# Performance work log

Measured on AMD Instinct MI355X. Metric: run time of the kernel, lower is better.

Reference implementation:

```python
import jax, jax.numpy as jnp
import numpy as np
from jax import lax

TAU = 0.1
N_ITERS = 20
B, N = 2048, 256


def setup_inputs() -> dict:
    key = jax.random.key(0)
    k1, k2 = jax.random.split(key)
    x = jax.random.normal(k1, (B, N), dtype=jnp.float32)
    x_norm = jax.random.normal(k2, (B, N), dtype=jnp.float32)
    reference_vec = jnp.linspace(-1.0, 1.0, N, dtype=jnp.float32)
    return {"x": x, "x_norm": x_norm, "reference_vec": reference_vec}


def reference(x, x_norm, reference_vec):
    # log_alpha: [B, N, N] = -|x_norm_i - ref_j| / tau
    log_alpha = -jnp.abs(x_norm[..., None] - reference_vec) / TAU

    def body(la, _):
        la = la - jax.nn.logsumexp(la, axis=-1, keepdims=True)  # row norm
        la = la - jax.nn.logsumexp(la, axis=-2, keepdims=True)  # col norm
        return la, None

    log_alpha, _ = lax.scan(body, log_alpha, None, length=N_ITERS)
    perm = jnp.exp(log_alpha)  # soft permutation [B, N, N]
    return jnp.einsum("bij,bj->bi", perm, x)
```

## Files before the change

### kernel.cpp

```cpp
#include <hip/hip_runtime.h>

#define NN 256
#define NITER 20
static constexpr float KK = 14.426950408889634f;

template<int CTRL, int RM>
__device__ __forceinline__ float dppadd(float x) {
  int v = __builtin_amdgcn_update_dpp(0, __float_as_int(x), CTRL, RM, 0xF, true);
  return x + __int_as_float(v);
}
template<int CTRL, int RM>
__device__ __forceinline__ int dppaddi(int x) {
  int v = __builtin_amdgcn_update_dpp(0, x, CTRL, RM, 0xF, true);
  return x + v;
}
__device__ __forceinline__ float rlane(float v, int l) {
  return __int_as_float(__builtin_amdgcn_readlane(__float_as_int(v), l));
}
__device__ __forceinline__ float rcpf(float x) {
  float r; asm("v_rcp_f32 %0, %1" : "=v"(r) : "v"(x)); return r;
}

__global__ __launch_bounds__(64)
void sinkhorn_wave(const float* __restrict__ x,
                   const float* __restrict__ xn,
                   const float* __restrict__ refv,
                   float* __restrict__ out)
{
  __shared__ __align__(16) float2   W[258];
  __shared__ __align__(16) unsigned hist[NN];
  __shared__ __align__(16) int      exclArr[NN];
  __shared__ __align__(16) float    xsArr[NN];
  __shared__ __align__(16) int      origArr[NN];

  const int lane = threadIdx.x;
  const int b = blockIdx.x;
  const int j4 = lane * 4;
  const size_t base = (size_t)b * NN;

  float xnv[4], xv[4], rv[4];
  { float4 t = *(const float4*)(xn + base + j4); xnv[0]=t.x; xnv[1]=t.y; xnv[2]=t.z; xnv[3]=t.w; }
  { float4 t = *(const float4*)(x  + base + j4); xv[0]=t.x;  xv[1]=t.y;  xv[2]=t.z;  xv[3]=t.w; }
  { float4 t = *(const float4*)(refv + j4);      rv[0]=t.x;  rv[1]=t.y;  rv[2]=t.z;  rv[3]=t.w; }

  *(uint4*)&hist[j4] = make_uint4(0u, 0u, 0u, 0u);
  float vc[4]; int cb[4]; unsigned rtn[4];
  #pragma unroll
  for (int t = 0; t < 4; ++t) {
    vc[t] = fminf(fmaxf(xnv[t], -1.0f), 1.0f);
    cb[t] = (int)fmaf(vc[t], 127.5f, 127.5f);
    rtn[t] = atomicAdd(&hist[cb[t]], 1u);
  }
  uint4 hv = *(uint4*)&hist[j4];
  int ih0 = (int)hv.x, ih1 = ih0 + (int)hv.y, ih2 = ih1 + (int)hv.z, ih3 = ih2 + (int)hv.w;
  int sH = ih3;
  sH = dppaddi<0x111, 0xF>(sH);
  sH = dppaddi<0x112, 0xF>(sH);
  sH = dppaddi<0x114, 0xF>(sH);
  sH = dppaddi<0x118, 0xF>(sH);
  sH = dppaddi<0x142, 0xA>(sH);
  sH = dppaddi<0x143, 0xC>(sH);
  const int offH = sH - ih3;
  int slotM[4] = { offH, offH + ih0, offH + ih1, offH + ih2 };
  *(int4*)&exclArr[j4] = make_int4(slotM[0], slotM[1], slotM[2], slotM[3]);
  #pragma unroll
  for (int t = 0; t < 4; ++t) {
    int slot = exclArr[cb[t]] + (int)rtn[t];
    xsArr[slot]   = vc[t];
    origArr[slot] = j4 + t;
  }
  float xs[4]; int orig[4];
  { float4 t = *(float4*)&xsArr[j4]; xs[0]=t.x; xs[1]=t.y; xs[2]=t.z; xs[3]=t.w; }
  { int4  t = *(int4*)&origArr[j4]; orig[0]=t.x; orig[1]=t.y; orig[2]=t.z; orig[3]=t.w; }

  int slotJ[4];
  #pragma unroll
  for (int t = 0; t < 4; ++t) slotJ[t] = (int)fmaf(xs[t], 127.5f, 127.5f) + 1;

  float Ep[4], Em[4], Epx[4], Emx[4];
  #pragma unroll
  for (int t = 0; t < 4; ++t) {
    Ep[t]  = exp2f( KK * rv[t]);  Em[t]  = exp2f(-KK * rv[t]);
    Epx[t] = exp2f( KK * xs[t]);  Emx[t] = exp2f(-KK * xs[t]);
  }

  auto scan_store = [&](float pa0, float pa1, float pa2, float pa3,
                        float qb0, float qb1, float qb2, float qb3) {
    float ip0 = pa0, ip1 = ip0 + pa1, ip2 = ip1 + pa2, ip3 = ip2 + pa3;
    float sq3 = qb3, sq2 = sq3 + qb2, sq1 = sq2 + qb1, sq0 = sq1 + qb0;
    float sP = ip3;
    sP = dppadd<0x111, 0xF>(sP);
    sP = dppadd<0x112, 0xF>(sP);
    sP = dppadd<0x114, 0xF>(sP);
    sP = dppadd<0x118, 0xF>(sP);
    sP = dppadd<0x142, 0xA>(sP);
    sP = dppadd<0x143, 0xC>(sP);
    float offP = sP - ip3;
    float sQ = sq0;
    sQ = dppadd<0x101, 0xF>(sQ);
    sQ = dppadd<0x102, 0xF>(sQ);
    sQ = dppadd<0x104, 0xF>(sQ);
    sQ = dppadd<0x108, 0xF>(sQ);
    float q1 = rlane(sQ, 16), q2 = rlane(sQ, 32), q3 = rlane(sQ, 48);
    int row = lane >> 4;
    float offQ = sQ - sq0;
    offQ += (row < 1) ? q1 : 0.f;
    offQ += (row < 2) ? q2 : 0.f;
    offQ += (row < 3) ? q3 : 0.f;
    float4 w0 = make_float4(offP,       offQ + sq0, offP + ip0, offQ + sq1);
    float4 w1 = make_float4(offP + ip1, offQ + sq2, offP + ip2, offQ + sq3);
    *(float4*)&W[j4]     = w0;
    *(float4*)&W[j4 + 2] = w1;
    if (lane == 63) W[256] = make_float2(sP, 0.f);
  };

  float vC[4] = {1.f, 1.f, 1.f, 1.f}, vR[4];
  #pragma unroll 1
  for (int it = 0; it < NITER; ++it) {
    scan_store(Ep[0]*vC[0], Ep[1]*vC[1], Ep[2]*vC[2], Ep[3]*vC[3],
               Em[0]*vC[0], Em[1]*vC[1], Em[2]*vC[2], Em[3]*vC[3]);
    #pragma unroll
    for (int t = 0; t < 4; ++t) {
      float2 w = W[slotJ[t]];
      vR[t] = rcpf(fmaf(Emx[t], w.x, Epx[t] * w.y));
    }
    scan_store(Epx[0]*vR[0], Epx[1]*vR[1], Epx[2]*vR[2], Epx[3]*vR[3],
               Emx[0]*vR[0], Emx[1]*vR[1], Emx[2]*vR[2], Emx[3]*vR[3]);
    #pragma unroll
    for (int t = 0; t < 4; ++t) {
      float2 w = W[slotM[t]];
      vC[t] = rcpf(fmaf(Em[t], w.x, Ep[t] * w.y));
    }
  }
  {
    float g0 = vC[0]*xv[0], g1 = vC[1]*xv[1], g2 = vC[2]*xv[2], g3 = vC[3]*xv[3];
    scan_store(Ep[0]*g0, Ep[1]*g1, Ep[2]*g2, Ep[3]*g3,
               Em[0]*g0, Em[1]*g1, Em[2]*g2, Em[3]*g3);
    #pragma unroll
    for (int t = 0; t < 4; ++t) {
      float2 w = W[slotJ[t]];
      float S = fmaf(Emx[t], w.x, Epx[t] * w.y);
      out[base + orig[t]] = vR[t] * S;
    }
  }
}

extern "C" void kernel_launch(void* const* d_in, const int* in_sizes, int n_in,
                              void* d_out, int out_size, void* d_ws, size_t ws_size,
                              hipStream_t stream) {
  const float* x    = (const float*)d_in[0];
  const float* xnrm = (const float*)d_in[1];
  const float* refv = (const float*)d_in[2];
  float* out = (float*)d_out;
  const int B = in_sizes[0] / NN;
  sinkhorn_wave<<<dim3(B), dim3(64), 0, stream>>>(x, xnrm, refv, out);
}
```

Before: 21.14 us.

## Merge reference and sample points into one sorted array to drop LDS gathers

Builds a single merged order of the 256 reference points and 256 sorted samples (512 entries, 8 per lane) using a doubled-key histogram. Each Sinkhorn half-pass then becomes one prefix scan over the merged array, with potentials updated in registers through a selector mask, so the per-iteration LDS store and gather of the scan table go away. This adds twice the per-lane arithmetic (8 elements instead of 4 with masked, redundant work) and more LDS setup. The output is written through an LDS staging buffer so the global store is coalesced.

New measurement: 24.29 us. +14.9%, slower.

```diff
diff --git a/kernel.cpp b/kernel.cpp
--- a/kernel.cpp
+++ b/kernel.cpp
@@ -2,7 +2,8 @@
 
 #define NN 256
 #define NITER 20
-static constexpr float KK = 14.426950408889634f;
+static constexpr float KK   = 14.426950408889634f;
+static constexpr float DREF = 2.0f / 255.0f;
 
 template<int CTRL, int RM>
 __device__ __forceinline__ float dppadd(float x) {
@@ -20,128 +21,169 @@
 __device__ __forceinline__ float rcpf(float x) {
   float r; asm("v_rcp_f32 %0, %1" : "=v"(r) : "v"(x)); return r;
 }
+__device__ __forceinline__ float wavescan(float t) {
+  float s = t;
+  s = dppadd<0x111,0xF>(s); s = dppadd<0x112,0xF>(s);
+  s = dppadd<0x114,0xF>(s); s = dppadd<0x118,0xF>(s);
+  s = dppadd<0x142,0xA>(s); s = dppadd<0x143,0xC>(s);
+  return s;
+}
 
 __global__ __launch_bounds__(64)
-void sinkhorn_wave(const float* __restrict__ x,
-                   const float* __restrict__ xn,
-                   const float* __restrict__ refv,
-                   float* __restrict__ out)
+void sinkhorn_merged(const float* __restrict__ x,
+                     const float* __restrict__ xn,
+                     const float* __restrict__ refv,
+                     float* __restrict__ out)
 {
-  __shared__ __align__(16) float2   W[258];
-  __shared__ __align__(16) unsigned hist[NN];
-  __shared__ __align__(16) int      exclArr[NN];
-  __shared__ __align__(16) float    xsArr[NN];
-  __shared__ __align__(16) int      origArr[NN];
+  __shared__ __align__(16) unsigned hist2[512];
+  __shared__ __align__(16) int      excl2[512];
+  __shared__ __align__(16) float2   AR[512];
+  __shared__ __align__(16) float2   AX[512];
+  __shared__ __align__(16) float2   WO[512];
+  __shared__ __align__(16) float    outA[NN];
 
   const int lane = threadIdx.x;
-  const int b = blockIdx.x;
-  const int j4 = lane * 4;
-  const size_t base = (size_t)b * NN;
+  const int j4 = lane * 4, j8 = lane * 8;
+  const size_t base = (size_t)blockIdx.x * NN;
 
   float xnv[4], xv[4], rv[4];
   { float4 t = *(const float4*)(xn + base + j4); xnv[0]=t.x; xnv[1]=t.y; xnv[2]=t.z; xnv[3]=t.w; }
   { float4 t = *(const float4*)(x  + base + j4); xv[0]=t.x;  xv[1]=t.y;  xv[2]=t.z;  xv[3]=t.w; }
   { float4 t = *(const float4*)(refv + j4);      rv[0]=t.x;  rv[1]=t.y;  rv[2]=t.z;  rv[3]=t.w; }
 
-  *(uint4*)&hist[j4] = make_uint4(0u, 0u, 0u, 0u);
-  float vc[4]; int cb[4]; unsigned rtn[4];
+  *(uint4*)&hist2[j8]     = make_uint4(0u,0u,0u,0u);
+  *(uint4*)&hist2[j8 + 4] = make_uint4(0u,0u,0u,0u);
+  int key[4]; unsigned rtn[4]; float vc[4];
   #pragma unroll
   for (int t = 0; t < 4; ++t) {
     vc[t] = fminf(fmaxf(xnv[t], -1.0f), 1.0f);
-    cb[t] = (int)fmaf(vc[t], 127.5f, 127.5f);
-    rtn[t] = atomicAdd(&hist[cb[t]], 1u);
+    int cb = (int)fmaf(vc[t], 127.5f, 127.5f);
+    int ge = (vc[t] >= fmaf((float)cb, DREF, -1.0f)) ? 1 : 0;
+    key[t] = 2 * cb + ge;
+    rtn[t] = atomicAdd(&hist2[key[t]], 1u);
   }
-  uint4 hv = *(uint4*)&hist[j4];
-  int ih0 = (int)hv.x, ih1 = ih0 + (int)hv.y, ih2 = ih1 + (int)hv.z, ih3 = ih2 + (int)hv.w;
-  int sH = ih3;
-  sH = dppaddi<0x111, 0xF>(sH);
-  sH = dppaddi<0x112, 0xF>(sH);
-  sH = dppaddi<0x114, 0xF>(sH);
-  sH = dppaddi<0x118, 0xF>(sH);
-  sH = dppaddi<0x142, 0xA>(sH);
-  sH = dppaddi<0x143, 0xC>(sH);
-  const int offH = sH - ih3;
-  int slotM[4] = { offH, offH + ih0, offH + ih1, offH + ih2 };
-  *(int4*)&exclArr[j4] = make_int4(slotM[0], slotM[1], slotM[2], slotM[3]);
+  uint4 h0 = *(uint4*)&hist2[j8];
+  uint4 h1 = *(uint4*)&hist2[j8 + 4];
+  int ie1 = (int)h0.x, ie2 = ie1 + (int)h0.y, ie3 = ie2 + (int)h0.z, ie4 = ie3 + (int)h0.w;
+  int ie5 = ie4 + (int)h1.x, ie6 = ie5 + (int)h1.y, ie7 = ie6 + (int)h1.z, th = ie7 + (int)h1.w;
+  int sH = th;
+  sH = dppaddi<0x111,0xF>(sH); sH = dppaddi<0x112,0xF>(sH);
+  sH = dppaddi<0x114,0xF>(sH); sH = dppaddi<0x118,0xF>(sH);
+  sH = dppaddi<0x142,0xA>(sH); sH = dppaddi<0x143,0xC>(sH);
+  const int offH = sH - th;
+  *(int4*)&excl2[j8]     = make_int4(offH, offH+ie1, offH+ie2, offH+ie3);
+  *(int4*)&excl2[j8 + 4] = make_int4(offH+ie4, offH+ie5, offH+ie6, offH+ie7);
+  const int ieOdd[4] = { ie1, ie3, ie5, ie7 };
+  int posR[4], posX[4];
+  #pragma unroll
+  for (int t = 0; t < 4; ++t) posR[t] = offH + ieOdd[t] + j4 + t;
+  #pragma unroll
+  for (int t = 0; t < 4; ++t) posX[t] = excl2[key[t]] + (int)rtn[t] + ((key[t] + 1) >> 1);
+
   #pragma unroll
   for (int t = 0; t < 4; ++t) {
-    int slot = exclArr[cb[t]] + (int)rtn[t];
-    xsArr[slot]   = vc[t];
-    origArr[slot] = j4 + t;
+    float rp = exp2f( KK * rv[t]), rm = exp2f(-KK * rv[t]);
+    float qp = exp2f( KK * vc[t]), qm = exp2f(-KK * vc[t]);
+    AR[posR[t]] = make_float2(rp, rm);
+    AX[posR[t]] = make_float2(0.f, 0.f);
+    WO[posR[t]] = make_float2(xv[t], 0.f);
+    AR[posX[t]] = make_float2(0.f, 0.f);
+    AX[posX[t]] = make_float2(qp, qm);
+    WO[posX[t]] = make_float2(0.f, __int_as_float(j4 + t));
   }
-  float xs[4]; int orig[4];
-  { float4 t = *(float4*)&xsArr[j4]; xs[0]=t.x; xs[1]=t.y; xs[2]=t.z; xs[3]=t.w; }
-  { int4  t = *(int4*)&origArr[j4]; orig[0]=t.x; orig[1]=t.y; orig[2]=t.z; orig[3]=t.w; }
+  float EpR[8], EmR[8], EpX[8], EmX[8], Epq[8], Emq[8], mX[8], mR[8], pot[8];
+  #pragma unroll
+  for (int i = 0; i < 8; i += 2) {
+    float4 r = *(float4*)&AR[j8 + i];
+    EpR[i] = r.x; EmR[i] = r.y; EpR[i+1] = r.z; EmR[i+1] = r.w;
+    float4 q = *(float4*)&AX[j8 + i];
+    EpX[i] = q.x; EmX[i] = q.y; EpX[i+1] = q.z; EmX[i+1] = q.w;
+  }
+  #pragma unroll
+  for (int i = 0; i < 8; ++i) {
+    Epq[i] = EpR[i] + EpX[i];  Emq[i] = EmR[i] + EmX[i];
+    mX[i] = (EpX[i] > 0.f) ? 1.f : 0.f;  mR[i] = 1.f - mX[i];
+    pot[i] = 1.f;
+  }
+  const int row = lane >> 4;
 
-  int slotJ[4];
-  #pragma unroll
-  for (int t = 0; t < 4; ++t) slotJ[t] = (int)fmaf(xs[t], 127.5f, 127.5f) + 1;
-
-  float Ep[4], Em[4], Epx[4], Emx[4];
-  #pragma unroll
-  for (int t = 0; t < 4; ++t) {
-    Ep[t]  = exp2f( KK * rv[t]);  Em[t]  = exp2f(-KK * rv[t]);
-    Epx[t] = exp2f( KK * xs[t]);  Emx[t] = exp2f(-KK * xs[t]);
-  }
-
-  auto scan_store = [&](float pa0, float pa1, float pa2, float pa3,
-                        float qb0, float qb1, float qb2, float qb3) {
-    float ip0 = pa0, ip1 = ip0 + pa1, ip2 = ip1 + pa2, ip3 = ip2 + pa3;
-    float sq3 = qb3, sq2 = sq3 + qb2, sq1 = sq2 + qb1, sq0 = sq1 + qb0;
-    float sP = ip3;
-    sP = dppadd<0x111, 0xF>(sP);
-    sP = dppadd<0x112, 0xF>(sP);
-    sP = dppadd<0x114, 0xF>(sP);
-    sP = dppadd<0x118, 0xF>(sP);
-    sP = dppadd<0x142, 0xA>(sP);
-    sP = dppadd<0x143, 0xC>(sP);
-    float offP = sP - ip3;
-    float sQ = sq0;
-    sQ = dppadd<0x101, 0xF>(sQ);
-    sQ = dppadd<0x102, 0xF>(sQ);
-    sQ = dppadd<0x104, 0xF>(sQ);
-    sQ = dppadd<0x108, 0xF>(sQ);
+  auto pass = [&](const float (&cp)[8], const float (&cm)[8], const float (&sel)[8]) {
+    float a[8], c[8], ea[8], sc[8], ta;
+    #pragma unroll
+    for (int i = 0; i < 8; ++i) { a[i] = cp[i] * pot[i]; c[i] = cm[i] * pot[i]; }
+    { float u01=a[0]+a[1], u23=a[2]+a[3], u03=u01+u23, u45=a[4]+a[5];
+      ea[0]=0.f; ea[1]=a[0]; ea[2]=u01; ea[3]=u01+a[2]; ea[4]=u03;
+      ea[5]=u03+a[4]; ea[6]=u03+u45; ea[7]=ea[6]+a[6]; ta=ea[7]+a[7]; }
+    sc[7]=c[7]; sc[6]=c[6]+sc[7]; sc[5]=c[5]+sc[6]; sc[4]=c[4]+sc[5];
+    sc[3]=c[3]+sc[4]; sc[2]=c[2]+sc[3]; sc[1]=c[1]+sc[2]; sc[0]=c[0]+sc[1];
+    const float tc = sc[0];
+    float sA = wavescan(ta);
+    float offA = sA - ta;
+    float sQ = tc;
+    sQ = dppadd<0x101,0xF>(sQ);
+    sQ = dppadd<0x102,0xF>(sQ);
+    sQ = dppadd<0x104,0xF>(sQ);
+    sQ = dppadd<0x108,0xF>(sQ);
     float q1 = rlane(sQ, 16), q2 = rlane(sQ, 32), q3 = rlane(sQ, 48);
-    int row = lane >> 4;
-    float offQ = sQ - sq0;
+    float offQ = sQ - tc;
     offQ += (row < 1) ? q1 : 0.f;
     offQ += (row < 2) ? q2 : 0.f;
     offQ += (row < 3) ? q3 : 0.f;
-    float4 w0 = make_float4(offP,       offQ + sq0, offP + ip0, offQ + sq1);
-    float4 w1 = make_float4(offP + ip1, offQ + sq2, offP + ip2, offQ + sq3);
-    *(float4*)&W[j4]     = w0;
-    *(float4*)&W[j4 + 2] = w1;
-    if (lane == 63) W[256] = make_float2(sP, 0.f);
+    #pragma unroll
+    for (int i = 0; i < 8; ++i) {
+      float A = offA + ea[i];
+      float D = offQ + sc[i];
+      float S = fmaf(Emq[i], A, Epq[i] * D);
+      float r = rcpf(S);
+      pot[i] = fmaf(sel[i], r - pot[i], pot[i]);
+    }
   };
 
-  float vC[4] = {1.f, 1.f, 1.f, 1.f}, vR[4];
   #pragma unroll 1
   for (int it = 0; it < NITER; ++it) {
-    scan_store(Ep[0]*vC[0], Ep[1]*vC[1], Ep[2]*vC[2], Ep[3]*vC[3],
-               Em[0]*vC[0], Em[1]*vC[1], Em[2]*vC[2], Em[3]*vC[3]);
+    pass(EpR, EmR, mX);
+    pass(EpX, EmX, mR);
+  }
+
+  {
+    float xw[8]; int og[8];
     #pragma unroll
-    for (int t = 0; t < 4; ++t) {
-      float2 w = W[slotJ[t]];
-      vR[t] = rcpf(fmaf(Emx[t], w.x, Epx[t] * w.y));
+    for (int i = 0; i < 8; i += 2) {
+      float4 w = *(float4*)&WO[j8 + i];
+      xw[i] = w.x; og[i] = __float_as_int(w.y);
+      xw[i+1] = w.z; og[i+1] = __float_as_int(w.w);
     }
-    scan_store(Epx[0]*vR[0], Epx[1]*vR[1], Epx[2]*vR[2], Epx[3]*vR[3],
-               Emx[0]*vR[0], Emx[1]*vR[1], Emx[2]*vR[2], Emx[3]*vR[3]);
+    float a[8], c[8], ea[8], sc[8], ta;
     #pragma unroll
-    for (int t = 0; t < 4; ++t) {
-      float2 w = W[slotM[t]];
-      vC[t] = rcpf(fmaf(Em[t], w.x, Ep[t] * w.y));
+    for (int i = 0; i < 8; ++i) { float g = xw[i] * pot[i]; a[i] = EpR[i] * g; c[i] = EmR[i] * g; }
+    { float u01=a[0]+a[1], u23=a[2]+a[3], u03=u01+u23, u45=a[4]+a[5];
+      ea[0]=0.f; ea[1]=a[0]; ea[2]=u01; ea[3]=u01+a[2]; ea[4]=u03;
+      ea[5]=u03+a[4]; ea[6]=u03+u45; ea[7]=ea[6]+a[6]; ta=ea[7]+a[7]; }
+    sc[7]=c[7]; sc[6]=c[6]+sc[7]; sc[5]=c[5]+sc[6]; sc[4]=c[4]+sc[5];
+    sc[3]=c[3]+sc[4]; sc[2]=c[2]+sc[3]; sc[1]=c[1]+sc[2]; sc[0]=c[0]+sc[1];
+    const float tc = sc[0];
+    float sA = wavescan(ta);
+    float offA = sA - ta;
+    float sQ = tc;
+    sQ = dppadd<0x101,0xF>(sQ);
+    sQ = dppadd<0x102,0xF>(sQ);
+    sQ = dppadd<0x104,0xF>(sQ);
+    sQ = dppadd<0x108,0xF>(sQ);
+    float q1 = rlane(sQ, 16), q2 = rlane(sQ, 32), q3 = rlane(sQ, 48);
+    float offQ = sQ - tc;
+    offQ += (row < 1) ? q1 : 0.f;
+    offQ += (row < 2) ? q2 : 0.f;
+    offQ += (row < 3) ? q3 : 0.f;
+    #pragma unroll
+    for (int i = 0; i < 8; ++i) {
+      float A = offA + ea[i];
+      float D = offQ + sc[i];
+      float S = fmaf(Emq[i], A, Epq[i] * D);
+      float val = pot[i] * S;
+      if (mX[i] != 0.f) outA[og[i]] = val;
     }
-  }
-  {
-    float g0 = vC[0]*xv[0], g1 = vC[1]*xv[1], g2 = vC[2]*xv[2], g3 = vC[3]*xv[3];
-    scan_store(Ep[0]*g0, Ep[1]*g1, Ep[2]*g2, Ep[3]*g3,
-               Em[0]*g0, Em[1]*g1, Em[2]*g2, Em[3]*g3);
-    #pragma unroll
-    for (int t = 0; t < 4; ++t) {
-      float2 w = W[slotJ[t]];
-      float S = fmaf(Emx[t], w.x, Epx[t] * w.y);
-      out[base + orig[t]] = vR[t] * S;
-    }
+    float4 o = *(float4*)&outA[j4];
+    *(float4*)(out + base + j4) = o;
   }
 }
 
@@ -153,5 +195,5 @@
   const float* refv = (const float*)d_in[2];
   float* out = (float*)d_out;
   const int B = in_sizes[0] / NN;
-  sinkhorn_wave<<<dim3(B), dim3(64), 0, stream>>>(x, xnrm, refv, out);
+  sinkhorn_merged<<<dim3(B), dim3(64), 0, stream>>>(x, xnrm, refv, out);
 }
```
